# Kernel optimization log

Hardware: AMD Instinct MI355X
Metric: run time of the kernel (lower is better)

The kernel has to match this reference:

```python
import jax, jax.numpy as jnp
import numpy as np

N_NODES = 100000


def gcn_layer(x, ei, W, b):
    # PyG GCNConv with add_self_loops=True, edge_weight=None (all ones)
    N = x.shape[0]
    loops = jnp.arange(N, dtype=ei.dtype)
    src = jnp.concatenate([ei[0], loops])
    dst = jnp.concatenate([ei[1], loops])
    h = x @ W  # [N, out_dim]
    ones = jnp.ones(src.shape[0], dtype=x.dtype)
    deg = jax.ops.segment_sum(ones, dst, num_segments=N)
    dinv = jnp.where(deg > 0, jax.lax.rsqrt(deg), 0.0)
    norm = dinv[src] * dinv[dst]  # [E+N]
    msgs = norm[:, None] * h[src]
    out = jax.ops.segment_sum(msgs, dst, num_segments=N)
    return out + b


def forward_once(x, ei, W1, b1, W2, b2):
    h = jax.nn.relu(gcn_layer(x, ei, W1, b1))
    # Dropout(0.25) is identity in eval mode
    z = gcn_layer(h, ei, W2, b2)
    return z  # [N, embed_dim]


def setup_inputs() -> dict:
    key = jax.random.key(0)
    k = jax.random.split(key, 6)
    feat_dim, hidden_dim, embed_dim = 128, 32, 16
    R, E = 4, 1600000
    x = jax.random.normal(k[0], (N_NODES, feat_dim), dtype=jnp.float32)
    eis = jax.random.randint(k[1], (R, 2, E), 0, N_NODES, dtype=jnp.int32)
    s1 = 1.0 / np.sqrt(feat_dim)
    s2 = 1.0 / np.sqrt(hidden_dim)
    W1 = jax.random.uniform(k[2], (feat_dim, hidden_dim), jnp.float32, -s1, s1)
    b1 = jax.random.uniform(k[3], (hidden_dim,), jnp.float32, -s1, s1)
    W2 = jax.random.uniform(k[4], (hidden_dim, embed_dim), jnp.float32, -s2, s2)
    b2 = jax.random.uniform(k[5], (embed_dim,), jnp.float32, -s2, s2)
    return {"x": x, "eis": eis, "W1": W1, "b1": b1, "W2": W2, "b2": b2}


def reference(x, eis, W1, b1, W2, b2):
    # vectorize the per-relation loop over the leading R axis of eis
    embeds = jax.vmap(lambda ei: forward_once(x, ei, W1, b1, W2, b2))(eis)
    # default reduce: embeds.sum(dim=2) on [R, N, embed_dim] -> [R, N]
    return embeds.sum(axis=2)
```

## Files before the change

kernel.cpp:

```cpp
#include <hip/hip_runtime.h>


constexpr int N    = 100000;
constexpr int E    = 1600000;
constexpr int R    = 4;
constexpr int FEAT = 128;
constexpr int HID  = 32;
constexpr int EMB  = 16;
constexpr int M    = R * N;
constexpr int BS   = 256;
constexpr int SH    = 9;
constexpr int BSPAN = 1 << SH;
constexpr int NBUCK = (N + BSPAN - 1) / BSPAN;
constexpr int CH    = 4096;
constexpr int EPT   = CH / BS;
constexpr int NBKr  = (E + CH - 1) / CH;
constexpr int RB    = R * NBUCK;
constexpr int CAP   = 8960;
constexpr int SPT   = (CAP + BSPAN - 1) / BSPAN;
constexpr int OCAP  = 1536;
constexpr int FIX   = 16;
constexpr int GNB   = 64;
constexpr int XPITCH = 132;

typedef _Float16 half8 __attribute__((ext_vector_type(8)));
typedef _Float16 half2v __attribute__((ext_vector_type(2)));

__global__ __launch_bounds__(BS)
void k_gemm_h0(const float* __restrict__ x, const float* __restrict__ W1,
               _Float16* __restrict__ H0h) {
    __shared__ float xs[GNB * XPITCH];
    int base = blockIdx.x * GNB;
    int tid  = threadIdx.x;
#pragma unroll
    for (int u = 0; u < 8; ++u) {
        int f = tid + u * BS;
        int n = f >> 5;
        int c = f & 31;
        if (base + n < N) {
            float4 v = ((const float4*)(x + (size_t)(base + n) * FEAT))[c];
            int p = c ^ ((n & 7) << 2);
            *(float4*)&xs[n * XPITCH + p * 4] = v;
        }
    }
    __syncthreads();
    int oct = __builtin_amdgcn_readfirstlane(tid >> 6);
    int l   = tid & 63;
    int i   = base + l;
    const float* wp = W1 + oct * 8;
    float acc[8];
#pragma unroll
    for (int kk = 0; kk < 8; ++kk) acc[kk] = 0.f;
#pragma unroll 4
    for (int c = 0; c < 32; ++c) {
        int p = c ^ ((l & 7) << 2);
        float4 xv = *(const float4*)&xs[l * XPITCH + p * 4];
        float xk[4] = {xv.x, xv.y, xv.z, xv.w};
#pragma unroll
        for (int dk = 0; dk < 4; ++dk) {
            const float* wr = wp + (c * 4 + dk) * HID;
#pragma unroll
            for (int j = 0; j < 8; ++j)
                acc[j] = fmaf(xk[dk], wr[j], acc[j]);
        }
    }
    half8 hv;
#pragma unroll
    for (int kk = 0; kk < 8; ++kk) hv[kk] = (_Float16)acc[kk];
    if (i < N) ((half8*)H0h)[i * 4 + oct] = hv;
}

__global__ void k_wrow(const float* __restrict__ W2, const float* __restrict__ b2,
                       float* __restrict__ wrowbuf, _Float16* __restrict__ Hsc) {
    int j = threadIdx.x;
    if (j < HID) {
        float s = 0.f;
#pragma unroll
        for (int k = 0; k < EMB; ++k) s += W2[j * EMB + k];
        wrowbuf[j] = s;
    } else if (j == HID) {
        float s = 0.f;
#pragma unroll
        for (int k = 0; k < EMB; ++k) s += b2[k];
        wrowbuf[HID] = s;
    } else if (j >= 34 && j < 50) {
        ((unsigned*)(Hsc + (size_t)M * HID))[j - 34] = 0u;
    }
}

__global__ void k_scat2(const int* __restrict__ eis, int* __restrict__ gcur,
                        int* __restrict__ binned) {
    __shared__ int hist[NBUCK], lstart[NBUCK], cursor[NBUCK], gbase[NBUCK];
    __shared__ int wpart[BS / 64];
    __shared__ int shuf[CH];
    __shared__ unsigned char bkt[CH];
    int r = blockIdx.x / NBKr, k = blockIdx.x - r * NBKr;
    const int* srcp = eis + (size_t)r * 2 * E;
    const int* dstp = srcp + E;
    int e0 = k * CH, n = min(CH, E - e0);
    int tid = threadIdx.x;

    int dreg[EPT], sreg[EPT];
    if (n == CH) {
#pragma unroll
        for (int u = 0; u < EPT; ++u) {
            dreg[u] = dstp[e0 + tid + u * BS];
            sreg[u] = srcp[e0 + tid + u * BS];
        }
    } else {
#pragma unroll
        for (int u = 0; u < EPT; ++u) {
            int i = tid + u * BS;
            dreg[u] = (i < n) ? dstp[e0 + i] : -1;
            sreg[u] = (i < n) ? srcp[e0 + i] : 0;
        }
    }
    for (int b = tid; b < NBUCK; b += BS) hist[b] = 0;
    __syncthreads();
#pragma unroll
    for (int u = 0; u < EPT; ++u)
        if (dreg[u] >= 0) atomicAdd(&hist[dreg[u] >> SH], 1);
    __syncthreads();
    int v = (tid < NBUCK) ? hist[tid] : 0;
    int lanei = tid & 63;
    int s = v;
#pragma unroll
    for (int d = 1; d < 64; d <<= 1) {
        int xup = __shfl_up(s, d, 64);
        s += (lanei >= d) ? xup : 0;
    }
    if (lanei == 63) wpart[tid >> 6] = s;
    __syncthreads();
    int offw = 0;
#pragma unroll
    for (int ww = 0; ww < BS / 64; ++ww)
        offw += (ww < (tid >> 6)) ? wpart[ww] : 0;
    int ex = offw + s - v;
    if (tid < NBUCK) {
        lstart[tid] = ex;
        cursor[tid] = ex;
        gbase[tid] = atomicAdd(&gcur[r * NBUCK + tid], v);
    }
    __syncthreads();
#pragma unroll
    for (int u = 0; u < EPT; ++u) {
        int d = dreg[u];
        if (d >= 0) {
            int b = d >> SH;
            int pos = atomicAdd(&cursor[b], 1);
            shuf[pos] = ((d & (BSPAN - 1)) << 17) | sreg[u];
            bkt[pos]  = (unsigned char)b;
        }
    }
    __syncthreads();
    if (n == CH) {
#pragma unroll
        for (int u = 0; u < EPT; ++u) {
            int i = tid + u * BS;
            int b = bkt[i];
            int pos = gbase[b] + (i - lstart[b]);
            if (pos < CAP)
                binned[(size_t)(r * NBUCK + b) * CAP + pos] = shuf[i];
        }
    } else {
        for (int i = tid; i < n; i += BS) {
            int b = bkt[i];
            int pos = gbase[b] + (i - lstart[b]);
            if (pos < CAP)
                binned[(size_t)(r * NBUCK + b) * CAP + pos] = shuf[i];
        }
    }
}

__global__ __launch_bounds__(BSPAN)
void k_sort3(const int* __restrict__ gcur, int* __restrict__ binned,
             int4* __restrict__ meta, const half8* __restrict__ H0h,
             half8* __restrict__ Hsc, int* __restrict__ fixedsrc) {
    __shared__ int fix_lds[FIX * BSPAN];
    __shared__ int hist[BSPAN], cur[BSPAN], oexs[BSPAN];
    __shared__ int wpart[BSPAN / 64];
    int gb = blockIdx.x;
    int r = gb / NBUCK, b = gb - r * NBUCK;
    int n = min(gcur[gb], CAP);
    int base = gb * CAP;
    int ovb  = base + (CAP - OCAP);
    int tid = threadIdx.x;
    int node = (b << SH) + tid;
    int ri = r * N + node;
    int nodec = min(node, N - 1);
    half8 h0r[4];
#pragma unroll
    for (int cc = 0; cc < 4; ++cc) h0r[cc] = H0h[(size_t)nodec * 4 + cc];
    int rg[SPT];
#pragma unroll
    for (int u = 0; u < SPT; ++u) {
        int i = tid + u * BSPAN;
        rg[u] = (i < n) ? binned[base + i] : -1;
    }
    hist[tid] = 0;
    cur[tid] = 0;
    __syncthreads();
#pragma unroll
    for (int u = 0; u < SPT; ++u)
        if (rg[u] >= 0) atomicAdd(&hist[((unsigned)rg[u]) >> 17], 1);
    __syncthreads();
    int v = hist[tid];
    int ov = max(v - FIX, 0);
    int lanei = tid & 63;
    int s = ov;
#pragma unroll
    for (int d = 1; d < 64; d <<= 1) {
        int xup = __shfl_up(s, d, 64);
        s += (lanei >= d) ? xup : 0;
    }
    if (lanei == 63) wpart[tid >> 6] = s;
    __syncthreads();
    int offw = 0;
#pragma unroll
    for (int ww = 0; ww < BSPAN / 64; ++ww)
        offw += (ww < (tid >> 6)) ? wpart[ww] : 0;
    int oex = offw + s - ov;
    oexs[tid] = oex;
    float di = rsqrtf((float)v + 1.0f);
    if (node < N) {
        int4 mw;
        mw.x = min(v, FIX + max(OCAP - oex, 0));
        mw.y = ovb + oex;
        mw.z = __float_as_int(di);
        mw.w = 0;
        meta[ri] = mw;
    }
    __syncthreads();
#pragma unroll
    for (int u = 0; u < SPT; ++u) {
        int rc = rg[u];
        if (rc >= 0) {
            int nd = ((unsigned)rc) >> 17;
            int k = atomicAdd(&cur[nd], 1);
            int val = rc & 0x1FFFF;
            if (k < FIX) {
                fix_lds[k * BSPAN + nd] = val;
            } else {
                int p = oexs[nd] + k - FIX;
                if (p < OCAP) binned[ovb + p] = val;
            }
        }
    }
    __syncthreads();
    if (node < N) {
        int nn = min(v, FIX);
#pragma unroll
        for (int cc = 0; cc < 4; ++cc) {
            int4 w;
            w.x = (cc * 4 + 0 < nn) ? fix_lds[(cc * 4 + 0) * BSPAN + tid] : 0;
            w.y = (cc * 4 + 1 < nn) ? fix_lds[(cc * 4 + 1) * BSPAN + tid] : 0;
            w.z = (cc * 4 + 2 < nn) ? fix_lds[(cc * 4 + 2) * BSPAN + tid] : 0;
            w.w = (cc * 4 + 3 < nn) ? fix_lds[(cc * 4 + 3) * BSPAN + tid] : 0;
            ((int4*)(fixedsrc + (size_t)ri * FIX))[cc] = w;
        }
#pragma unroll
        for (int cc = 0; cc < 4; ++cc) {
            half8 h = h0r[cc];
            half8 o;
#pragma unroll
            for (int kk = 0; kk < 8; ++kk) o[kk] = (_Float16)(di * (float)h[kk]);
            Hsc[(size_t)ri * 4 + cc] = o;
        }
    }
}

__global__ void k_l1(const int4* __restrict__ meta, const int* __restrict__ ssrc,
                     const int* __restrict__ fixedsrc, const half8* __restrict__ Hsc,
                     const float* __restrict__ b1, const float* __restrict__ wrowbuf,
                     float* __restrict__ q) {
    int t = blockIdx.x * blockDim.x + threadIdx.x;
    int ri = t >> 4;
    if (ri >= M) return;
    int lane = t & 15;
    int c   = lane & 3;
    int sub = lane >> 2;
    int i = ri % N;
    int rbase = ri - i;
    int fs = fixedsrc[(size_t)ri * FIX + lane];
    half8 hs = Hsc[(size_t)ri * 4 + c];
    int4 mo = meta[ri];
    int n = mo.x;
    int base = mo.y - FIX;
    float di = __int_as_float(mo.z);
    half2v acc[4];
    half2v zz = {(_Float16)0.f, (_Float16)0.f};
#pragma unroll
    for (int kk = 0; kk < 4; ++kk) acc[kk] = zz;

    auto procwin = [&](int sbv, int m) {
        for (int bq = 0; bq < 4 && bq * 4 < m; ++bq) {
            int slot = bq * 4 + sub;
            int sj = __shfl(sbv, slot, 16);
            int idx = (slot < m) ? (rbase + sj) : M;
            half8 h = Hsc[(size_t)idx * 4 + c];
#pragma unroll
            for (int kk = 0; kk < 4; ++kk) {
                half2v hp = {h[2 * kk], h[2 * kk + 1]};
                acc[kk] = acc[kk] + hp;
            }
        }
    };

    int sb = (16 + lane < n) ? ssrc[base + 16 + lane] : 0;
    procwin(fs, n);
    for (int k0 = 16; k0 < n; k0 += 16) {
        int sbn = (k0 + 16 + lane < n) ? ssrc[base + k0 + 16 + lane] : 0;
        procwin(sb, n - k0);
        sb = sbn;
    }
#pragma unroll
    for (int o = 4; o <= 8; o <<= 1) {
#pragma unroll
        for (int kk = 0; kk < 4; ++kk) {
            int av = __builtin_bit_cast(int, acc[kk]);
            av = __shfl_xor(av, o, 16);
            acc[kk] = acc[kk] + __builtin_bit_cast(half2v, av);
        }
    }
#pragma unroll
    for (int kk = 0; kk < 4; ++kk) {
        half2v hp = {hs[2 * kk], hs[2 * kk + 1]};
        acc[kk] = acc[kk] + hp;
    }
    float p = 0.f;
#pragma unroll
    for (int kk = 0; kk < 8; ++kk) {
        float av = (float)acc[kk >> 1][kk & 1];
        int j = c * 8 + kk;
        float h1 = fmaf(di, av, b1[j]);
        h1 = fmaxf(h1, 0.f);
        p = fmaf(h1, wrowbuf[j], p);
    }
    p += __shfl_xor(p, 1, 16);
    p += __shfl_xor(p, 2, 16);
    if (lane == 0) q[ri] = di * p;
}

__global__ void k_l2(const int4* __restrict__ meta, const int* __restrict__ ssrc,
                     const int* __restrict__ fixedsrc, const float* __restrict__ q,
                     const float* __restrict__ wrowbuf, float* __restrict__ out) {
    int t = blockIdx.x * blockDim.x + threadIdx.x;
    int ri = t >> 3;
    if (ri >= M) return;
    int lane = t & 7;
    int i = ri % N;
    int rbase = ri - i;
    int f0 = fixedsrc[(size_t)ri * FIX + lane];
    int f1 = fixedsrc[(size_t)ri * FIX + 8 + lane];
    int4 mo = meta[ri];
    int n = mo.x;
    int base = mo.y - FIX;
    float val = 0.f;
    if (lane < n)     val += q[rbase + f0];
    if (8 + lane < n) val += q[rbase + f1];
    for (int idx = 16 + lane; idx < n; idx += 8) {
        int s = ssrc[base + idx];
        val += q[rbase + s];
    }
#pragma unroll
    for (int o = 4; o > 0; o >>= 1) val += __shfl_xor(val, o, 8);
    if (lane == 0)
        out[ri] = __int_as_float(mo.z) * (val + q[ri]) + wrowbuf[HID];
}

extern "C" void kernel_launch(void* const* d_in, const int* in_sizes, int n_in,
                              void* d_out, int out_size, void* d_ws, size_t ws_size,
                              hipStream_t stream) {
    const float* x  = (const float*)d_in[0];
    const int*  eis = (const int*)d_in[1];
    const float* W1 = (const float*)d_in[2];
    const float* b1 = (const float*)d_in[3];
    const float* W2 = (const float*)d_in[4];
    const float* b2 = (const float*)d_in[5];
    float* out = (float*)d_out;

    _Float16* H0h = (_Float16*)d_ws;
    float* q      = (float*)d_ws + (size_t)N * HID / 2;
    int4*  meta   = (int4*)(q + M);
    float* wrowbuf = (float*)(meta + M);
    int*   gcur   = (int*)(wrowbuf + 64);
    int*   binned = gcur + RB;
    _Float16* Hsc = (_Float16*)(binned + (size_t)RB * CAP);
    int* fixedsrc = (int*)(Hsc + (size_t)(M + 1) * HID);

    k_gemm_h0<<<(N + GNB - 1) / GNB, BS, 0, stream>>>(x, W1, H0h);
    k_wrow  <<<1, 64, 0, stream>>>(W2, b2, wrowbuf, Hsc);
    hipMemsetAsync(gcur, 0, (size_t)RB * sizeof(int), stream);
    k_scat2 <<<R * NBKr, BS, 0, stream>>>(eis, gcur, binned);
    k_sort3 <<<RB, BSPAN, 0, stream>>>(gcur, binned, meta,
                                       (const half8*)H0h, (half8*)Hsc, fixedsrc);
    k_l1    <<<(M * 16 + BS - 1) / BS, BS, 0, stream>>>(meta, binned, fixedsrc,
                                                        (const half8*)Hsc, b1,
                                                        wrowbuf, q);
    k_l2    <<<(M * 8 + BS - 1) / BS, BS, 0, stream>>>(meta, binned, fixedsrc,
                                                       q, wrowbuf, out);
}
```

Measured before the change: 306.5 us.

## Split layer-1 feature gather into two half-width passes over separate arrays

The scaled hidden features are split into two 16-channel fp16 arrays, and the layer-1 aggregation kernel runs twice, once per half. Each pass gathers 32-byte rows instead of 64-byte rows, so the working set per pass (about 12.8 MB) is more likely to fit in cache during random neighbor gathers. The first pass writes partial dot products to a new buffer that the second pass adds in. The cost is that the edge index lists, metadata and fixed-source arrays are read twice, plus one extra kernel launch.

```diff
diff --git a/kernel.cpp b/kernel.cpp
--- a/kernel.cpp
+++ b/kernel.cpp
@@ -24,6 +24,7 @@
 constexpr int XPITCH = 132;
 
 typedef _Float16 half8 __attribute__((ext_vector_type(8)));
+typedef _Float16 half4 __attribute__((ext_vector_type(4)));
 typedef _Float16 half2v __attribute__((ext_vector_type(2)));
 
 __global__ __launch_bounds__(BS)
@@ -71,7 +72,8 @@
 }
 
 __global__ void k_wrow(const float* __restrict__ W2, const float* __restrict__ b2,
-                       float* __restrict__ wrowbuf, _Float16* __restrict__ Hsc) {
+                       float* __restrict__ wrowbuf, _Float16* __restrict__ HscA,
+                       _Float16* __restrict__ HscB) {
     int j = threadIdx.x;
     if (j < HID) {
         float s = 0.f;
@@ -83,8 +85,10 @@
 #pragma unroll
         for (int k = 0; k < EMB; ++k) s += b2[k];
         wrowbuf[HID] = s;
-    } else if (j >= 34 && j < 50) {
-        ((unsigned*)(Hsc + (size_t)M * HID))[j - 34] = 0u;
+    } else if (j >= 34 && j < 42) {
+        ((unsigned*)(HscA + (size_t)M * 16))[j - 34] = 0u;
+    } else if (j >= 42 && j < 50) {
+        ((unsigned*)(HscB + (size_t)M * 16))[j - 42] = 0u;
     }
 }
 
@@ -175,7 +179,8 @@
 __global__ __launch_bounds__(BSPAN)
 void k_sort3(const int* __restrict__ gcur, int* __restrict__ binned,
              int4* __restrict__ meta, const half8* __restrict__ H0h,
-             half8* __restrict__ Hsc, int* __restrict__ fixedsrc) {
+             half8* __restrict__ HscA, half8* __restrict__ HscB,
+             int* __restrict__ fixedsrc) {
     __shared__ int fix_lds[FIX * BSPAN];
     __shared__ int hist[BSPAN], cur[BSPAN], oexs[BSPAN];
     __shared__ int wpart[BSPAN / 64];
@@ -264,15 +269,17 @@
             half8 o;
 #pragma unroll
             for (int kk = 0; kk < 8; ++kk) o[kk] = (_Float16)(di * (float)h[kk]);
-            Hsc[(size_t)ri * 4 + cc] = o;
-        }
-    }
-}
-
+            if (cc < 2) HscA[(size_t)ri * 2 + cc] = o;
+            else        HscB[(size_t)ri * 2 + (cc - 2)] = o;
+        }
+    }
+}
+
+template<int PASS>
 __global__ void k_l1(const int4* __restrict__ meta, const int* __restrict__ ssrc,
-                     const int* __restrict__ fixedsrc, const half8* __restrict__ Hsc,
+                     const int* __restrict__ fixedsrc, const half4* __restrict__ Hp,
                      const float* __restrict__ b1, const float* __restrict__ wrowbuf,
-                     float* __restrict__ q) {
+                     float* __restrict__ qp, float* __restrict__ q) {
     int t = blockIdx.x * blockDim.x + threadIdx.x;
     int ri = t >> 4;
     if (ri >= M) return;
@@ -282,27 +289,26 @@
     int i = ri % N;
     int rbase = ri - i;
     int fs = fixedsrc[(size_t)ri * FIX + lane];
-    half8 hs = Hsc[(size_t)ri * 4 + c];
+    half4 hs = Hp[(size_t)ri * 4 + c];
+    float pprev = (PASS == 1) ? qp[ri] : 0.f;
     int4 mo = meta[ri];
     int n = mo.x;
     int base = mo.y - FIX;
     float di = __int_as_float(mo.z);
-    half2v acc[4];
+    half2v acc[2];
     half2v zz = {(_Float16)0.f, (_Float16)0.f};
-#pragma unroll
-    for (int kk = 0; kk < 4; ++kk) acc[kk] = zz;
+    acc[0] = zz; acc[1] = zz;
 
     auto procwin = [&](int sbv, int m) {
         for (int bq = 0; bq < 4 && bq * 4 < m; ++bq) {
             int slot = bq * 4 + sub;
             int sj = __shfl(sbv, slot, 16);
             int idx = (slot < m) ? (rbase + sj) : M;
-            half8 h = Hsc[(size_t)idx * 4 + c];
-#pragma unroll
-            for (int kk = 0; kk < 4; ++kk) {
-                half2v hp = {h[2 * kk], h[2 * kk + 1]};
-                acc[kk] = acc[kk] + hp;
-            }
+            half4 h = Hp[(size_t)idx * 4 + c];
+            half2v h0 = {h[0], h[1]};
+            half2v h1 = {h[2], h[3]};
+            acc[0] = acc[0] + h0;
+            acc[1] = acc[1] + h1;
         }
     };
 
@@ -316,29 +322,33 @@
 #pragma unroll
     for (int o = 4; o <= 8; o <<= 1) {
 #pragma unroll
-        for (int kk = 0; kk < 4; ++kk) {
+        for (int kk = 0; kk < 2; ++kk) {
             int av = __builtin_bit_cast(int, acc[kk]);
             av = __shfl_xor(av, o, 16);
             acc[kk] = acc[kk] + __builtin_bit_cast(half2v, av);
         }
     }
+    {
+        half2v h0 = {hs[0], hs[1]};
+        half2v h1 = {hs[2], hs[3]};
+        acc[0] = acc[0] + h0;
+        acc[1] = acc[1] + h1;
+    }
+    float p = 0.f;
 #pragma unroll
     for (int kk = 0; kk < 4; ++kk) {
-        half2v hp = {hs[2 * kk], hs[2 * kk + 1]};
-        acc[kk] = acc[kk] + hp;
-    }
-    float p = 0.f;
-#pragma unroll
-    for (int kk = 0; kk < 8; ++kk) {
         float av = (float)acc[kk >> 1][kk & 1];
-        int j = c * 8 + kk;
+        int j = PASS * 16 + c * 4 + kk;
         float h1 = fmaf(di, av, b1[j]);
         h1 = fmaxf(h1, 0.f);
         p = fmaf(h1, wrowbuf[j], p);
     }
     p += __shfl_xor(p, 1, 16);
     p += __shfl_xor(p, 2, 16);
-    if (lane == 0) q[ri] = di * p;
+    if (lane == 0) {
+        if (PASS == 0) qp[ri] = p;
+        else           q[ri] = di * (p + pprev);
+    }
 }
 
 __global__ void k_l2(const int4* __restrict__ meta, const int* __restrict__ ssrc,
@@ -381,22 +391,27 @@
 
     _Float16* H0h = (_Float16*)d_ws;
     float* q      = (float*)d_ws + (size_t)N * HID / 2;
-    int4*  meta   = (int4*)(q + M);
+    float* qp     = q + M;
+    int4*  meta   = (int4*)(qp + M);
     float* wrowbuf = (float*)(meta + M);
     int*   gcur   = (int*)(wrowbuf + 64);
     int*   binned = gcur + RB;
-    _Float16* Hsc = (_Float16*)(binned + (size_t)RB * CAP);
-    int* fixedsrc = (int*)(Hsc + (size_t)(M + 1) * HID);
+    _Float16* HscA = (_Float16*)(binned + (size_t)RB * CAP);
+    _Float16* HscB = HscA + (size_t)(M + 1) * 16;
+    int* fixedsrc = (int*)(HscB + (size_t)(M + 1) * 16);
 
     k_gemm_h0<<<(N + GNB - 1) / GNB, BS, 0, stream>>>(x, W1, H0h);
-    k_wrow  <<<1, 64, 0, stream>>>(W2, b2, wrowbuf, Hsc);
+    k_wrow  <<<1, 64, 0, stream>>>(W2, b2, wrowbuf, HscA, HscB);
     hipMemsetAsync(gcur, 0, (size_t)RB * sizeof(int), stream);
     k_scat2 <<<R * NBKr, BS, 0, stream>>>(eis, gcur, binned);
-    k_sort3 <<<RB, BSPAN, 0, stream>>>(gcur, binned, meta,
-                                       (const half8*)H0h, (half8*)Hsc, fixedsrc);
-    k_l1    <<<(M * 16 + BS - 1) / BS, BS, 0, stream>>>(meta, binned, fixedsrc,
-                                                        (const half8*)Hsc, b1,
-                                                        wrowbuf, q);
+    k_sort3 <<<RB, BSPAN, 0, stream>>>(gcur, binned, meta, (const half8*)H0h,
+                                       (half8*)HscA, (half8*)HscB, fixedsrc);
+    k_l1<0> <<<(M * 16 + BS - 1) / BS, BS, 0, stream>>>(meta, binned, fixedsrc,
+                                                        (const half4*)HscA, b1,
+                                                        wrowbuf, qp, q);
+    k_l1<1> <<<(M * 16 + BS - 1) / BS, BS, 0, stream>>>(meta, binned, fixedsrc,
+                                                        (const half4*)HscB, b1,
+                                                        wrowbuf, qp, q);
     k_l2    <<<(M * 8 + BS - 1) / BS, BS, 0, stream>>>(meta, binned, fixedsrc,
                                                        q, wrowbuf, out);
 }
```

Result: slower. 335.6 us (+9.5%).
